# Kernel tuning notes

Measured on AMD Instinct MI355X. Metric: run time of the kernel, lower is better.

## Reference

```python
import jax, jax.numpy as jnp
import numpy as np

D = 1024      # hidden_size
H = 16        # num_attention_heads
HD = D // H   # head dim
F = 4096      # ffn_size
EPS_MHA = 1e-8   # LayerNorm inside MultiHeadAttention (its default)
EPS_ENC = 1e-6   # EncoderLayer LayerNorms


def layer_norm(x, gamma, beta, eps):
    mu = jnp.mean(x, axis=-1, keepdims=True)
    var = jnp.mean(jnp.square(x - mu), axis=-1, keepdims=True)
    return (x - mu) * jax.lax.rsqrt(var + eps) * gamma + beta


def setup_inputs() -> dict:
    key = jax.random.key(0)
    ks = jax.random.split(key, 16)
    B, S = 8, 1024
    s = 0.02
    inp = {
        "query": jax.random.normal(ks[0], (B, S, D), jnp.float32),
        "key": jax.random.normal(ks[1], (B, S, D), jnp.float32),
        "value": jax.random.normal(ks[2], (B, S, D), jnp.float32),
        "attention_mask": jnp.ones((B, 1, 1, S), jnp.float32),
        # MHA projection weights
        "wq": jax.random.normal(ks[3], (D, D), jnp.float32) * s,
        "bq": jnp.zeros((D,), jnp.float32),
        "wk": jax.random.normal(ks[4], (D, D), jnp.float32) * s,
        "bk": jnp.zeros((D,), jnp.float32),
        "wv": jax.random.normal(ks[5], (D, D), jnp.float32) * s,
        "bv": jnp.zeros((D,), jnp.float32),
        "wo": jax.random.normal(ks[6], (D, D), jnp.float32) * s,
        "bo": jnp.zeros((D,), jnp.float32),
        "ln_mha_g": jnp.ones((D,), jnp.float32),
        "ln_mha_b": jnp.zeros((D,), jnp.float32),
        # FFN
        "w1": jax.random.normal(ks[7], (D, F), jnp.float32) * s,
        "b1": jnp.zeros((F,), jnp.float32),
        "w2": jax.random.normal(ks[8], (F, D), jnp.float32) * s,
        "b2": jnp.zeros((D,), jnp.float32),
        "ln_attn_g": jnp.ones((D,), jnp.float32),
        "ln_attn_b": jnp.zeros((D,), jnp.float32),
        "ln_ffn_g": jnp.ones((D,), jnp.float32),
        "ln_ffn_b": jnp.zeros((D,), jnp.float32),
    }
    return inp


def encoder_layer(query, key, value, attention_mask,
                  wq, bq, wk, bk, wv, bv, wo, bo, ln_mha_g, ln_mha_b,
                  w1, b1, w2, b2, ln_attn_g, ln_attn_b, ln_ffn_g, ln_ffn_b):
    B, S, _ = query.shape

    def split_heads(x):  # [B,S,D] -> [B,H,S,HD]
        return x.reshape(B, S, H, HD).transpose(0, 2, 1, 3)

    q = split_heads(query @ wq + bq)
    k = split_heads(key @ wk + bk)
    v = split_heads(value @ wv + bv)

    # scaled dot-product attention (full NxN scores, as in the original)
    score = jnp.einsum('bhqd,bhkd->bhqk', q, k) / jnp.sqrt(jnp.float32(HD))
    score = score + (1.0 - attention_mask) * -10000.0
    attn_weights = jax.nn.softmax(score, axis=-1)  # dropout inactive (inference)
    context = jnp.einsum('bhqk,bhkd->bhqd', attn_weights, v)
    context = context.transpose(0, 2, 1, 3).reshape(B, S, D)

    # MHA output proj + residual (w.r.t. original query) + its own LayerNorm
    attn_out = layer_norm(context @ wo + bo + query, ln_mha_g, ln_mha_b, EPS_MHA)

    # EncoderLayer: second residual add of query, then LayerNorm
    attn_out = layer_norm(query + attn_out, ln_attn_g, ln_attn_b, EPS_ENC)

    ffn = jax.nn.relu(attn_out @ w1 + b1) @ w2 + b2
    out = layer_norm(ffn + attn_out, ln_ffn_g, ln_ffn_b, EPS_ENC)
    return out, attn_weights


def reference(query, key, value, attention_mask,
              wq, bq, wk, bk, wv, bv, wo, bo, ln_mha_g, ln_mha_b,
              w1, b1, w2, b2, ln_attn_g, ln_attn_b, ln_ffn_g, ln_ffn_b):
    return encoder_layer(query, key, value, attention_mask,
                         wq, bq, wk, bk, wv, bv, wo, bo, ln_mha_g, ln_mha_b,
                         w1, b1, w2, b2, ln_attn_g, ln_attn_b, ln_ffn_g, ln_ffn_b)
```

## Files before the change

kernel.cpp:

```cpp
#include <hip/hip_runtime.h>

#define DEV __device__ __forceinline__

typedef __bf16 bf16x8 __attribute__((ext_vector_type(8)));
typedef unsigned short ushort8v __attribute__((ext_vector_type(8)));
typedef float floatx4 __attribute__((ext_vector_type(4)));

DEV unsigned short f2bf(float f) {
  unsigned int u = __float_as_uint(f);
  u += 0x7fffu + ((u >> 16) & 1u);
  return (unsigned short)(u >> 16);
}

__global__ __launch_bounds__(256) void cast_bf16_kernel(
    const float* __restrict__ in, unsigned short* __restrict__ out, int n4) {
  int i = blockIdx.x * 256 + threadIdx.x;
  if (i >= n4) return;
  float4 v = ((const float4*)in)[i];
  ushort4 o;
  o.x = f2bf(v.x); o.y = f2bf(v.y); o.z = f2bf(v.z); o.w = f2bf(v.w);
  ((ushort4*)out)[i] = o;
}

__global__ __launch_bounds__(256) void transpose_cast_kernel(
    const float* __restrict__ in, unsigned short* __restrict__ out, int R, int C) {
  __shared__ float tile[32][33];
  int c0 = blockIdx.x * 32, r0 = blockIdx.y * 32;
  int tx = threadIdx.x, ty = threadIdx.y;
#pragma unroll
  for (int j = 0; j < 32; j += 8)
    tile[ty + j][tx] = in[(long)(r0 + ty + j) * C + (c0 + tx)];
  __syncthreads();
#pragma unroll
  for (int j = 0; j < 32; j += 8)
    out[(long)(c0 + ty + j) * R + (r0 + tx)] = f2bf(tile[tx][ty + j]);
}

enum GemmMode { M_QPROJ = 0, M_KPROJ, M_VPROJ, M_SCORES, M_CTX, M_OPROJ, M_FFN1, M_FFN2 };

template <int MODE, int WM, int WN>
__global__ __launch_bounds__(WM * WN * 64)
void gemm_nt(const void* __restrict__ Ap, const unsigned short* __restrict__ Bp,
             const float* __restrict__ bias, void* __restrict__ Cp,
             const float* __restrict__ mask, int K, int ldA, int ldB,
             long zsA, long zsB) {
  constexpr int BM = WM * 64, BN = WN * 64, BK = 32, LDK = 40;
  constexpr int NT = WM * WN * 64;
  constexpr bool A_F32 = (MODE == M_CTX);
  __shared__ unsigned short As[BM * LDK];
  __shared__ unsigned short Bs[BN * LDK];

  const int tid = threadIdx.x;
  const int z = blockIdx.z;
  const long bm = (long)blockIdx.y * BM;
  const long bn = (long)blockIdx.x * BN;

  const float* Af = nullptr;
  const unsigned short* Ab = nullptr;
  if constexpr (A_F32) Af = (const float*)Ap + (long)z * zsA + bm * ldA;
  else                 Ab = (const unsigned short*)Ap + (long)z * zsA + bm * ldA;
  const unsigned short* B = Bp + (long)z * zsB + bn * ldB;

  const int wave = tid >> 6, lane = tid & 63;
  const int wn = wave % WN, wm = wave / WN;
  const int lr = lane & 15, kq = lane >> 4;

  floatx4 acc[4][4];
#pragma unroll
  for (int mt = 0; mt < 4; ++mt)
#pragma unroll
    for (int nt = 0; nt < 4; ++nt) acc[mt][nt] = floatx4{0.f, 0.f, 0.f, 0.f};

  for (int k0 = 0; k0 < K; k0 += BK) {
    __syncthreads();
#pragma unroll
    for (int c = tid; c < BM * 4; c += NT) {
      int r = c >> 2, kc = (c & 3) << 3;
      unsigned short* dst = &As[r * LDK + kc];
      if constexpr (A_F32) {
        const float* src = Af + (long)r * ldA + k0 + kc;
        float4 v0 = *(const float4*)src;
        float4 v1 = *(const float4*)(src + 4);
        ushort4 a{f2bf(v0.x), f2bf(v0.y), f2bf(v0.z), f2bf(v0.w)};
        ushort4 b{f2bf(v1.x), f2bf(v1.y), f2bf(v1.z), f2bf(v1.w)};
        *(ushort4*)dst = a;
        *(ushort4*)(dst + 4) = b;
      } else {
        *(ushort8v*)dst = *(const ushort8v*)(Ab + (long)r * ldA + k0 + kc);
      }
    }
#pragma unroll
    for (int c = tid; c < BN * 4; c += NT) {
      int r = c >> 2, kc = (c & 3) << 3;
      *(ushort8v*)&Bs[r * LDK + kc] = *(const ushort8v*)(B + (long)r * ldB + k0 + kc);
    }
    __syncthreads();

    bf16x8 af[4], bfr[4];
#pragma unroll
    for (int mt = 0; mt < 4; ++mt)
      af[mt] = *(const bf16x8*)&As[(wm * 64 + mt * 16 + lr) * LDK + kq * 8];
#pragma unroll
    for (int nt = 0; nt < 4; ++nt)
      bfr[nt] = *(const bf16x8*)&Bs[(wn * 64 + nt * 16 + lr) * LDK + kq * 8];
#pragma unroll
    for (int mt = 0; mt < 4; ++mt)
#pragma unroll
      for (int nt = 0; nt < 4; ++nt)
        acc[mt][nt] = __builtin_amdgcn_mfma_f32_16x16x32_bf16(af[mt], bfr[nt], acc[mt][nt], 0, 0, 0);
  }

#pragma unroll
  for (int mt = 0; mt < 4; ++mt) {
#pragma unroll
    for (int nt = 0; nt < 4; ++nt) {
#pragma unroll
      for (int i = 0; i < 4; ++i) {
        long gm = bm + wm * 64 + mt * 16 + kq * 4 + i;
        long gn = bn + wn * 64 + nt * 16 + lr;
        float v = acc[mt][nt][i];
        if constexpr (MODE == M_QPROJ || MODE == M_KPROJ) {
          v += bias[gn];
          if constexpr (MODE == M_QPROJ) v *= 0.125f;
          long b = gm >> 10, s = gm & 1023, h = gn >> 6, hd = gn & 63;
          ((unsigned short*)Cp)[((b * 16 + h) << 16) + (s << 6) + hd] = f2bf(v);
        } else if constexpr (MODE == M_VPROJ) {
          v += bias[gn];
          long b = gm >> 10, s = gm & 1023, h = gn >> 6, hd = gn & 63;
          ((unsigned short*)Cp)[((b * 16 + h) << 16) + (hd << 10) + s] = f2bf(v);
        } else if constexpr (MODE == M_SCORES) {
          v += (1.0f - mask[(long)(z >> 4) * 1024 + gn]) * -10000.0f;
          ((float*)Cp)[(long)z * 1048576 + gm * 1024 + gn] = v;
        } else if constexpr (MODE == M_CTX) {
          long b = z >> 4, h = z & 15;
          ((unsigned short*)Cp)[((b * 1024 + gm) << 10) + (h << 6) + gn] = f2bf(v);
        } else if constexpr (MODE == M_OPROJ || MODE == M_FFN2) {
          ((float*)Cp)[gm * 1024 + gn] = v + bias[gn];
        } else if constexpr (MODE == M_FFN1) {
          ((unsigned short*)Cp)[gm * 4096 + gn] = f2bf(fmaxf(v + bias[gn], 0.f));
        }
      }
    }
  }
}

__global__ __launch_bounds__(256) void softmax_kernel(float* __restrict__ p) {
  long row = blockIdx.x;
  float* x = p + (row << 10);
  int t = threadIdx.x, wid = t >> 6, lane = t & 63;
  float4 v = ((float4*)x)[t];
  float m = fmaxf(fmaxf(v.x, v.y), fmaxf(v.z, v.w));
#pragma unroll
  for (int o = 32; o > 0; o >>= 1) m = fmaxf(m, __shfl_down(m, o));
  __shared__ float sm[4], ss[4];
  if (lane == 0) sm[wid] = m;
  __syncthreads();
  m = fmaxf(fmaxf(sm[0], sm[1]), fmaxf(sm[2], sm[3]));
  v.x = __expf(v.x - m); v.y = __expf(v.y - m);
  v.z = __expf(v.z - m); v.w = __expf(v.w - m);
  float s = v.x + v.y + v.z + v.w;
#pragma unroll
  for (int o = 32; o > 0; o >>= 1) s += __shfl_down(s, o);
  if (lane == 0) ss[wid] = s;
  __syncthreads();
  s = ss[0] + ss[1] + ss[2] + ss[3];
  float r = 1.0f / s;
  v.x *= r; v.y *= r; v.z *= r; v.w *= r;
  ((float4*)x)[t] = v;
}

DEV void block_reduce2(float& s, float& s2, float* buf) {
  int wid = threadIdx.x >> 6, lane = threadIdx.x & 63;
#pragma unroll
  for (int o = 32; o > 0; o >>= 1) { s += __shfl_down(s, o); s2 += __shfl_down(s2, o); }
  if (lane == 0) { buf[wid] = s; buf[4 + wid] = s2; }
  __syncthreads();
  s = buf[0] + buf[1] + buf[2] + buf[3];
  s2 = buf[4] + buf[5] + buf[6] + buf[7];
  __syncthreads();
}

__global__ __launch_bounds__(256)
void ln_mha_kernel(const float* __restrict__ proj, const float* __restrict__ query,
                   const float* __restrict__ g1, const float* __restrict__ b1,
                   const float* __restrict__ g2, const float* __restrict__ b2,
                   float* __restrict__ attn_out, unsigned short* __restrict__ attn_out_bf) {
  __shared__ float buf[8];
  long row = blockIdx.x;
  int t = threadIdx.x;
  float4 a = ((const float4*)(proj + (row << 10)))[t];
  float4 q = ((const float4*)(query + (row << 10)))[t];
  float4 x{a.x + q.x, a.y + q.y, a.z + q.z, a.w + q.w};
  float s = x.x + x.y + x.z + x.w;
  float s2 = x.x * x.x + x.y * x.y + x.z * x.z + x.w * x.w;
  block_reduce2(s, s2, buf);
  float mu = s * (1.f / 1024.f);
  float inv = rsqrtf(fmaxf(s2 * (1.f / 1024.f) - mu * mu, 0.f) + 1e-8f);
  float4 g = ((const float4*)g1)[t], bb = ((const float4*)b1)[t];
  float4 y{(x.x - mu) * inv * g.x + bb.x, (x.y - mu) * inv * g.y + bb.y,
           (x.z - mu) * inv * g.z + bb.z, (x.w - mu) * inv * g.w + bb.w};
  float4 x2{q.x + y.x, q.y + y.y, q.z + y.z, q.w + y.w};
  s = x2.x + x2.y + x2.z + x2.w;
  s2 = x2.x * x2.x + x2.y * x2.y + x2.z * x2.z + x2.w * x2.w;
  block_reduce2(s, s2, buf);
  mu = s * (1.f / 1024.f);
  inv = rsqrtf(fmaxf(s2 * (1.f / 1024.f) - mu * mu, 0.f) + 1e-6f);
  g = ((const float4*)g2)[t]; bb = ((const float4*)b2)[t];
  float4 o{(x2.x - mu) * inv * g.x + bb.x, (x2.y - mu) * inv * g.y + bb.y,
           (x2.z - mu) * inv * g.z + bb.z, (x2.w - mu) * inv * g.w + bb.w};
  ((float4*)(attn_out + (row << 10)))[t] = o;
  ushort4 ob{f2bf(o.x), f2bf(o.y), f2bf(o.z), f2bf(o.w)};
  ((ushort4*)(attn_out_bf + (row << 10)))[t] = ob;
}

__global__ __launch_bounds__(256)
void ln_final_kernel(const float* __restrict__ ffn, const float* __restrict__ res,
                     const float* __restrict__ g1, const float* __restrict__ b1,
                     float* __restrict__ out) {
  __shared__ float buf[8];
  long row = blockIdx.x;
  int t = threadIdx.x;
  float4 a = ((const float4*)(ffn + (row << 10)))[t];
  float4 q = ((const float4*)(res + (row << 10)))[t];
  float4 x{a.x + q.x, a.y + q.y, a.z + q.z, a.w + q.w};
  float s = x.x + x.y + x.z + x.w;
  float s2 = x.x * x.x + x.y * x.y + x.z * x.z + x.w * x.w;
  block_reduce2(s, s2, buf);
  float mu = s * (1.f / 1024.f);
  float inv = rsqrtf(fmaxf(s2 * (1.f / 1024.f) - mu * mu, 0.f) + 1e-6f);
  float4 g = ((const float4*)g1)[t], bb = ((const float4*)b1)[t];
  float4 o{(x.x - mu) * inv * g.x + bb.x, (x.y - mu) * inv * g.y + bb.y,
           (x.z - mu) * inv * g.z + bb.z, (x.w - mu) * inv * g.w + bb.w};
  ((float4*)(out + (row << 10)))[t] = o;
}

extern "C" void kernel_launch(void* const* d_in, const int* in_sizes, int n_in,
                              void* d_out, int out_size, void* d_ws, size_t ws_size,
                              hipStream_t stream) {
  const float* query = (const float*)d_in[0];
  const float* key   = (const float*)d_in[1];
  const float* value = (const float*)d_in[2];
  const float* mask  = (const float*)d_in[3];
  const float* wq = (const float*)d_in[4];  const float* bq = (const float*)d_in[5];
  const float* wk = (const float*)d_in[6];  const float* bk = (const float*)d_in[7];
  const float* wv = (const float*)d_in[8];  const float* bv = (const float*)d_in[9];
  const float* wo = (const float*)d_in[10]; const float* bo = (const float*)d_in[11];
  const float* ln_mha_g = (const float*)d_in[12]; const float* ln_mha_b = (const float*)d_in[13];
  const float* w1 = (const float*)d_in[14]; const float* b1 = (const float*)d_in[15];
  const float* w2 = (const float*)d_in[16]; const float* b2 = (const float*)d_in[17];
  const float* ln_attn_g = (const float*)d_in[18]; const float* ln_attn_b = (const float*)d_in[19];
  const float* ln_ffn_g = (const float*)d_in[20];  const float* ln_ffn_b = (const float*)d_in[21];

  unsigned short* Xq  = (unsigned short*)d_ws;
  unsigned short* Xk  = Xq + 8388608;
  unsigned short* Xv  = Xk + 8388608;
  unsigned short* Qh  = Xv + 8388608;
  unsigned short* Hid = (unsigned short*)d_ws;
  unsigned short* Kh  = Qh + 8388608;
  unsigned short* VhT = Kh + 8388608;
  unsigned short* WqT = VhT + 8388608;
  unsigned short* WkT = WqT + 1048576;
  unsigned short* WvT = WkT + 1048576;
  unsigned short* WoT = WvT + 1048576;
  unsigned short* W1T = WoT + 1048576;
  unsigned short* W2T = W1T + 4194304;
  unsigned short* Ctx = W2T + 4194304;
  float* tmp1    = (float*)(Ctx + 8388608);
  float* AttnOut = tmp1 + 8388608;
  unsigned short* AttnOutBf = (unsigned short*)(AttnOut + 8388608);

  float* attnF = (float*)d_out + 8388608;
  float* outF  = (float*)d_out;

  cast_bf16_kernel<<<8192, 256, 0, stream>>>(query, Xq, 2097152);
  cast_bf16_kernel<<<8192, 256, 0, stream>>>(key,   Xk, 2097152);
  cast_bf16_kernel<<<8192, 256, 0, stream>>>(value, Xv, 2097152);
  transpose_cast_kernel<<<dim3(32, 32), dim3(32, 8), 0, stream>>>(wq, WqT, 1024, 1024);
  transpose_cast_kernel<<<dim3(32, 32), dim3(32, 8), 0, stream>>>(wk, WkT, 1024, 1024);
  transpose_cast_kernel<<<dim3(32, 32), dim3(32, 8), 0, stream>>>(wv, WvT, 1024, 1024);
  transpose_cast_kernel<<<dim3(32, 32), dim3(32, 8), 0, stream>>>(wo, WoT, 1024, 1024);
  transpose_cast_kernel<<<dim3(128, 32), dim3(32, 8), 0, stream>>>(w1, W1T, 1024, 4096);
  transpose_cast_kernel<<<dim3(32, 128), dim3(32, 8), 0, stream>>>(w2, W2T, 4096, 1024);
  gemm_nt<M_QPROJ, 2, 2><<<dim3(8, 64, 1), 256, 0, stream>>>(Xq, WqT, bq, Qh, nullptr, 1024, 1024, 1024, 0, 0);
  gemm_nt<M_KPROJ, 2, 2><<<dim3(8, 64, 1), 256, 0, stream>>>(Xk, WkT, bk, Kh, nullptr, 1024, 1024, 1024, 0, 0);
  gemm_nt<M_VPROJ, 2, 2><<<dim3(8, 64, 1), 256, 0, stream>>>(Xv, WvT, bv, VhT, nullptr, 1024, 1024, 1024, 0, 0);
  gemm_nt<M_SCORES, 2, 2><<<dim3(8, 8, 128), 256, 0, stream>>>(Qh, Kh, nullptr, attnF, mask, 64, 64, 64, 65536L, 65536L);
  softmax_kernel<<<131072, 256, 0, stream>>>(attnF);
  gemm_nt<M_CTX, 2, 1><<<dim3(1, 8, 128), 128, 0, stream>>>(attnF, VhT, nullptr, Ctx, nullptr, 1024, 1024, 1024, 1048576L, 65536L);
  gemm_nt<M_OPROJ, 2, 2><<<dim3(8, 64, 1), 256, 0, stream>>>(Ctx, WoT, bo, tmp1, nullptr, 1024, 1024, 1024, 0, 0);
  ln_mha_kernel<<<8192, 256, 0, stream>>>(tmp1, query, ln_mha_g, ln_mha_b, ln_attn_g, ln_attn_b, AttnOut, AttnOutBf);
  gemm_nt<M_FFN1, 2, 2><<<dim3(32, 64, 1), 256, 0, stream>>>(AttnOutBf, W1T, b1, Hid, nullptr, 1024, 1024, 1024, 0, 0);
  gemm_nt<M_FFN2, 2, 2><<<dim3(8, 64, 1), 256, 0, stream>>>(Hid, W2T, b2, tmp1, nullptr, 4096, 4096, 4096, 0, 0);
  ln_final_kernel<<<8192, 256, 0, stream>>>(tmp1, AttnOut, ln_ffn_g, ln_ffn_b, outF);
}
```

Before: 1.765 ms.

## Fuse scores, softmax and context GEMM into one two-pass attention kernel

Replaces the scores GEMM, the standalone softmax and the context GEMM with a single fused kernel. Each block handles 128 query rows of one head. A first pass over K computes running row max and sum, and a second pass recomputes the scores, writes the normalized fp32 probabilities once, and multiplies bf16 probabilities by V from LDS. This removes the write-read-write-read round trips of the 512MB fp32 score matrix, at the cost of computing QK^T twice and issuing scattered scalar fp32 probability stores.

```diff
diff --git a/kernel.cpp b/kernel.cpp
--- a/kernel.cpp
+++ b/kernel.cpp
@@ -144,29 +144,194 @@
   }
 }
 
-__global__ __launch_bounds__(256) void softmax_kernel(float* __restrict__ p) {
-  long row = blockIdx.x;
-  float* x = p + (row << 10);
-  int t = threadIdx.x, wid = t >> 6, lane = t & 63;
-  float4 v = ((float4*)x)[t];
-  float m = fmaxf(fmaxf(v.x, v.y), fmaxf(v.z, v.w));
-#pragma unroll
-  for (int o = 32; o > 0; o >>= 1) m = fmaxf(m, __shfl_down(m, o));
-  __shared__ float sm[4], ss[4];
-  if (lane == 0) sm[wid] = m;
+__global__ __launch_bounds__(256) void attn_fused_kernel(
+    const unsigned short* __restrict__ Qh, const unsigned short* __restrict__ Kh,
+    const unsigned short* __restrict__ VhT, const float* __restrict__ mask,
+    float* __restrict__ probs, unsigned short* __restrict__ Ctx) {
+  constexpr int LDK = 72;
+  constexpr int LDP = 136;
+  __shared__ unsigned short Klds[128 * LDK];
+  __shared__ unsigned short Ps[128 * LDP];
+
+  int bid = blockIdx.x;
+  int orig = (bid & 7) * 128 + (bid >> 3);
+  const int z = orig >> 3, qb = orig & 7;
+
+  const long zoff = (long)z << 16;
+  const unsigned short* Qp = Qh + zoff + ((long)qb << 13);
+  const unsigned short* Kp = Kh + zoff;
+  const unsigned short* Vp = VhT + zoff;
+  const float* mrow = mask + (long)(z >> 4) * 1024;
+  float* prow = probs + ((long)z << 20) + ((long)qb << 17);
+
+  const int tid = threadIdx.x;
+  const int wave = tid >> 6, lane = tid & 63;
+  const int wm = wave >> 1, wn = wave & 1;
+  const int lr = lane & 15, kq = lane >> 4;
+
+  bf16x8 qf[4][2];
+#pragma unroll
+  for (int mt = 0; mt < 4; ++mt)
+#pragma unroll
+    for (int ks = 0; ks < 2; ++ks)
+      qf[mt][ks] = *(const bf16x8*)(Qp + (wm * 64 + mt * 16 + lr) * 64 + ks * 32 + kq * 8);
+
+  float m_run[4][4], l_run[4][4];
+#pragma unroll
+  for (int mt = 0; mt < 4; ++mt)
+#pragma unroll
+    for (int i = 0; i < 4; ++i) { m_run[mt][i] = -3.0e38f; l_run[mt][i] = 0.f; }
+
+  for (int c = 0; c < 8; ++c) {
+    __syncthreads();
+#pragma unroll
+    for (int cc = tid; cc < 1024; cc += 256) {
+      int r = cc >> 3, kc = (cc & 7) << 3;
+      *(ushort8v*)&Klds[r * LDK + kc] = *(const ushort8v*)(Kp + ((c << 7) + r) * 64 + kc);
+    }
+    __syncthreads();
+    bf16x8 kf[2][4];
+#pragma unroll
+    for (int ks = 0; ks < 2; ++ks)
+#pragma unroll
+      for (int nt = 0; nt < 4; ++nt)
+        kf[ks][nt] = *(const bf16x8*)&Klds[(wn * 64 + nt * 16 + lr) * LDK + ks * 32 + kq * 8];
+    float mk[4];
+#pragma unroll
+    for (int nt = 0; nt < 4; ++nt)
+      mk[nt] = (1.0f - mrow[(c << 7) + wn * 64 + nt * 16 + lr]) * -10000.0f;
+#pragma unroll
+    for (int mt = 0; mt < 4; ++mt) {
+      floatx4 a[4];
+#pragma unroll
+      for (int nt = 0; nt < 4; ++nt) a[nt] = floatx4{0.f, 0.f, 0.f, 0.f};
+#pragma unroll
+      for (int ks = 0; ks < 2; ++ks)
+#pragma unroll
+        for (int nt = 0; nt < 4; ++nt)
+          a[nt] = __builtin_amdgcn_mfma_f32_16x16x32_bf16(qf[mt][ks], kf[ks][nt], a[nt], 0, 0, 0);
+#pragma unroll
+      for (int i = 0; i < 4; ++i) {
+        float s0 = a[0][i] + mk[0], s1 = a[1][i] + mk[1];
+        float s2 = a[2][i] + mk[2], s3 = a[3][i] + mk[3];
+        float tm = fmaxf(fmaxf(s0, s1), fmaxf(s2, s3));
+#pragma unroll
+        for (int o = 1; o < 16; o <<= 1) tm = fmaxf(tm, __shfl_xor(tm, o));
+        float mn = fmaxf(m_run[mt][i], tm);
+        float ps = __expf(s0 - mn) + __expf(s1 - mn) + __expf(s2 - mn) + __expf(s3 - mn);
+#pragma unroll
+        for (int o = 1; o < 16; o <<= 1) ps += __shfl_xor(ps, o);
+        l_run[mt][i] = l_run[mt][i] * __expf(m_run[mt][i] - mn) + ps;
+        m_run[mt][i] = mn;
+      }
+    }
+  }
+
   __syncthreads();
-  m = fmaxf(fmaxf(sm[0], sm[1]), fmaxf(sm[2], sm[3]));
-  v.x = __expf(v.x - m); v.y = __expf(v.y - m);
-  v.z = __expf(v.z - m); v.w = __expf(v.w - m);
-  float s = v.x + v.y + v.z + v.w;
-#pragma unroll
-  for (int o = 32; o > 0; o >>= 1) s += __shfl_down(s, o);
-  if (lane == 0) ss[wid] = s;
+  float* mred = (float*)Klds;
+  float* lred = mred + 256;
+  if (lr == 0) {
+#pragma unroll
+    for (int mt = 0; mt < 4; ++mt)
+#pragma unroll
+      for (int i = 0; i < 4; ++i) {
+        int r = wm * 64 + mt * 16 + kq * 4 + i;
+        mred[wn * 128 + r] = m_run[mt][i];
+        lred[wn * 128 + r] = l_run[mt][i];
+      }
+  }
   __syncthreads();
-  s = ss[0] + ss[1] + ss[2] + ss[3];
-  float r = 1.0f / s;
-  v.x *= r; v.y *= r; v.z *= r; v.w *= r;
-  ((float4*)x)[t] = v;
+  float rl[4][4];
+#pragma unroll
+  for (int mt = 0; mt < 4; ++mt)
+#pragma unroll
+    for (int i = 0; i < 4; ++i) {
+      int r = wm * 64 + mt * 16 + kq * 4 + i;
+      float m0 = mred[r], m1 = mred[128 + r];
+      float l0 = lred[r], l1 = lred[128 + r];
+      float mm = fmaxf(m0, m1);
+      float ll = l0 * __expf(m0 - mm) + l1 * __expf(m1 - mm);
+      m_run[mt][i] = mm;
+      rl[mt][i] = 1.0f / ll;
+    }
+
+  floatx4 cacc[4][2];
+#pragma unroll
+  for (int mt = 0; mt < 4; ++mt)
+#pragma unroll
+    for (int n2 = 0; n2 < 2; ++n2) cacc[mt][n2] = floatx4{0.f, 0.f, 0.f, 0.f};
+
+  for (int c = 0; c < 8; ++c) {
+    __syncthreads();
+#pragma unroll
+    for (int cc = tid; cc < 1024; cc += 256) {
+      int r = cc >> 3, kc = (cc & 7) << 3;
+      *(ushort8v*)&Klds[r * LDK + kc] = *(const ushort8v*)(Kp + ((c << 7) + r) * 64 + kc);
+    }
+    __syncthreads();
+    bf16x8 kf[2][4];
+#pragma unroll
+    for (int ks = 0; ks < 2; ++ks)
+#pragma unroll
+      for (int nt = 0; nt < 4; ++nt)
+        kf[ks][nt] = *(const bf16x8*)&Klds[(wn * 64 + nt * 16 + lr) * LDK + ks * 32 + kq * 8];
+    float mk[4];
+#pragma unroll
+    for (int nt = 0; nt < 4; ++nt)
+      mk[nt] = (1.0f - mrow[(c << 7) + wn * 64 + nt * 16 + lr]) * -10000.0f;
+#pragma unroll
+    for (int mt = 0; mt < 4; ++mt) {
+      floatx4 a[4];
+#pragma unroll
+      for (int nt = 0; nt < 4; ++nt) a[nt] = floatx4{0.f, 0.f, 0.f, 0.f};
+#pragma unroll
+      for (int ks = 0; ks < 2; ++ks)
+#pragma unroll
+        for (int nt = 0; nt < 4; ++nt)
+          a[nt] = __builtin_amdgcn_mfma_f32_16x16x32_bf16(qf[mt][ks], kf[ks][nt], a[nt], 0, 0, 0);
+#pragma unroll
+      for (int nt = 0; nt < 4; ++nt) {
+#pragma unroll
+        for (int i = 0; i < 4; ++i) {
+          float p = __expf(a[nt][i] + mk[nt] - m_run[mt][i]) * rl[mt][i];
+          int row = wm * 64 + mt * 16 + kq * 4 + i;
+          int col = wn * 64 + nt * 16 + lr;
+          prow[(long)row * 1024 + (c << 7) + col] = p;
+          Ps[row * LDP + (col ^ (kq << 4))] = f2bf(p);
+        }
+      }
+    }
+    __syncthreads();
+#pragma unroll
+    for (int k2 = 0; k2 < 4; ++k2) {
+      bf16x8 pa[4], vb[2];
+#pragma unroll
+      for (int mt = 0; mt < 4; ++mt) {
+        int row = wm * 64 + mt * 16 + lr;
+        pa[mt] = *(const bf16x8*)&Ps[row * LDP + ((k2 * 32 + kq * 8) ^ ((lr >> 2) << 4))];
+      }
+#pragma unroll
+      for (int n2 = 0; n2 < 2; ++n2)
+        vb[n2] = *(const bf16x8*)(Vp + (wn * 32 + n2 * 16 + lr) * 1024 + (c << 7) + k2 * 32 + kq * 8);
+#pragma unroll
+      for (int mt = 0; mt < 4; ++mt)
+#pragma unroll
+        for (int n2 = 0; n2 < 2; ++n2)
+          cacc[mt][n2] = __builtin_amdgcn_mfma_f32_16x16x32_bf16(pa[mt], vb[n2], cacc[mt][n2], 0, 0, 0);
+    }
+  }
+
+  const int b = z >> 4, h = z & 15;
+#pragma unroll
+  for (int mt = 0; mt < 4; ++mt)
+#pragma unroll
+    for (int n2 = 0; n2 < 2; ++n2)
+#pragma unroll
+      for (int i = 0; i < 4; ++i) {
+        long srow = (long)b * 1024 + qb * 128 + wm * 64 + mt * 16 + kq * 4 + i;
+        int hd = wn * 32 + n2 * 16 + lr;
+        Ctx[(srow << 10) + (h << 6) + hd] = f2bf(cacc[mt][n2][i]);
+      }
 }
 
 DEV void block_reduce2(float& s, float& s2, float* buf) {
@@ -284,9 +449,7 @@
   gemm_nt<M_QPROJ, 2, 2><<<dim3(8, 64, 1), 256, 0, stream>>>(Xq, WqT, bq, Qh, nullptr, 1024, 1024, 1024, 0, 0);
   gemm_nt<M_KPROJ, 2, 2><<<dim3(8, 64, 1), 256, 0, stream>>>(Xk, WkT, bk, Kh, nullptr, 1024, 1024, 1024, 0, 0);
   gemm_nt<M_VPROJ, 2, 2><<<dim3(8, 64, 1), 256, 0, stream>>>(Xv, WvT, bv, VhT, nullptr, 1024, 1024, 1024, 0, 0);
-  gemm_nt<M_SCORES, 2, 2><<<dim3(8, 8, 128), 256, 0, stream>>>(Qh, Kh, nullptr, attnF, mask, 64, 64, 64, 65536L, 65536L);
-  softmax_kernel<<<131072, 256, 0, stream>>>(attnF);
-  gemm_nt<M_CTX, 2, 1><<<dim3(1, 8, 128), 128, 0, stream>>>(attnF, VhT, nullptr, Ctx, nullptr, 1024, 1024, 1024, 1048576L, 65536L);
+  attn_fused_kernel<<<1024, 256, 0, stream>>>(Qh, Kh, VhT, mask, attnF, Ctx);
   gemm_nt<M_OPROJ, 2, 2><<<dim3(8, 64, 1), 256, 0, stream>>>(Ctx, WoT, bo, tmp1, nullptr, 1024, 1024, 1024, 0, 0);
   ln_mha_kernel<<<8192, 256, 0, stream>>>(tmp1, query, ln_mha_g, ln_mha_b, ln_attn_g, ln_attn_b, AttnOut, AttnOutBf);
   gemm_nt<M_FFN1, 2, 2><<<dim3(32, 64, 1), 256, 0, stream>>>(AttnOutBf, W1T, b1, Hid, nullptr, 1024, 1024, 1024, 0, 0);
```

New measurement: 1.519 ms. 1.16x faster.
